# Optimization experiments

Measured on AMD Instinct MI355X. Metric: run time of the kernel, lower is better.

The kernel has to match this reference:

```python
import jax, jax.numpy as jnp
import numpy as np

D_MODEL = 1024
NUM_HEADS = 16
D_K = D_MODEL // NUM_HEADS
B, S = 1, 4096


def setup_inputs() -> dict:
    key = jax.random.key(0)
    ks = jax.random.split(key, 11)
    std = 1.0 / np.sqrt(D_MODEL)
    def lin(k):
        kw, kb = jax.random.split(k)
        W = jax.random.uniform(kw, (D_MODEL, D_MODEL), jnp.float32, -std, std)
        b = jax.random.uniform(kb, (D_MODEL,), jnp.float32, -std, std)
        return W, b
    Wq, bq = lin(ks[0]); Wk, bk = lin(ks[1]); Wv, bv = lin(ks[2]); Wo, bo = lin(ks[3])
    q = jax.random.normal(ks[4], (B, S, D_MODEL), jnp.float32)
    k = jax.random.normal(ks[5], (B, S, D_MODEL), jnp.float32)
    v = jax.random.normal(ks[6], (B, S, D_MODEL), jnp.float32)
    return {"q": q, "k": k, "v": v,
            "Wq": Wq, "bq": bq, "Wk": Wk, "bk": bk,
            "Wv": Wv, "bv": bv, "Wo": Wo, "bo": bo}


def reference(q, k, v, Wq, bq, Wk, bk, Wv, bv, Wo, bo):
    Bq, Sq, _ = q.shape
    # Linear projections (torch Linear: x @ W.T + b)
    def split_heads(x):
        return x.reshape(Bq, -1, NUM_HEADS, D_K).transpose(0, 2, 1, 3)  # [B,H,S,Dk]
    query = split_heads(q @ Wq.T + bq)
    key_ = split_heads(k @ Wk.T + bk)
    value = split_heads(v @ Wv.T + bv)
    scores = jnp.einsum('bhsd,bhtd->bhst', query, key_) / jnp.sqrt(jnp.float32(D_K))
    attn = jax.nn.softmax(scores, axis=-1)  # [B,H,S,S]
    ctx = jnp.einsum('bhst,bhtd->bhsd', attn, value)
    ctx = ctx.transpose(0, 2, 1, 3).reshape(Bq, Sq, NUM_HEADS * D_K)
    return ctx @ Wo.T + bo
```

## Files before the change

### kernel.cpp

```cpp
#include <hip/hip_runtime.h>
#include <cstdint>
#include <cstddef>

#define S_LEN 4096
#define DMODEL 1024
#define NHEADS 16
#define DK 64
#define ACT (S_LEN * DMODEL)
#define WELE (DMODEL * DMODEL)

typedef __bf16 bf16;
typedef bf16  bf16x4 __attribute__((ext_vector_type(4)));
typedef bf16  bf16x8 __attribute__((ext_vector_type(8)));
typedef float f32x4  __attribute__((ext_vector_type(4)));

__device__ __forceinline__ void async16(const void* g, void* l) {
    __builtin_amdgcn_global_load_lds(
        (__attribute__((address_space(1))) void*)(uintptr_t)g,
        (__attribute__((address_space(3))) void*)(uintptr_t)l,
        16, 0, 0);
}

__device__ __forceinline__ float fast_exp2(float x) {
#if __has_builtin(__builtin_amdgcn_exp2f)
    return __builtin_amdgcn_exp2f(x);
#else
    return exp2f(x);
#endif
}

__global__ void __launch_bounds__(256) cvt7(
    const float* a0, const float* a1, const float* a2,
    const float* w0, const float* w1, const float* w2, const float* w3,
    bf16* oa0, bf16* oa1, bf16* oa2,
    bf16* ow0, bf16* ow1, bf16* ow2, bf16* ow3,
    int nA, int nB)
{
    const float* s; bf16* d; int n4;
    switch (blockIdx.y) {
        case 0: s = a0; d = oa0; n4 = nA; break;
        case 1: s = a1; d = oa1; n4 = nA; break;
        case 2: s = a2; d = oa2; n4 = nA; break;
        case 3: s = w0; d = ow0; n4 = nB; break;
        case 4: s = w1; d = ow1; n4 = nB; break;
        case 5: s = w2; d = ow2; n4 = nB; break;
        default: s = w3; d = ow3; n4 = nB; break;
    }
    int i = blockIdx.x * 256 + threadIdx.x;
    if (i < n4) {
        float4 v = ((const float4*)s)[i];
        bf16x4 r = { (bf16)v.x, (bf16)v.y, (bf16)v.z, (bf16)v.w };
        ((bf16x4*)d)[i] = r;
    }
}

__device__ __forceinline__ void gemm_core_128x128(
    const bf16* __restrict__ A, const bf16* __restrict__ B,
    bf16* As, bf16* Bs, f32x4 (&acc)[4][4],
    int m0, int n0, int wm, int wn, int K)
{
    const int tid  = threadIdx.x;
    const int wave = tid >> 6;
    const int lane = tid & 63;
    const int quad = lane >> 4;
    const int l16  = lane & 15;

    const int srow = tid >> 2;
    const int scol = (tid & 3) * 8;
    const bf16* Ag = A + (size_t)(m0 + srow) * K + scol;
    const bf16* Bg = B + (size_t)(n0 + srow) * K + scol;
    char* lA = (char*)As + wave * 1024;
    char* lB = (char*)Bs + wave * 1024;

    for (int k0 = 0; k0 < K; k0 += 32) {
        async16(Ag,                  lA);
        async16(Ag + (size_t)64 * K, lA + 4096);
        async16(Bg,                  lB);
        async16(Bg + (size_t)64 * K, lB + 4096);
        Ag += 32; Bg += 32;
        __syncthreads();

        bf16x8 af[4], bfr[4];
#pragma unroll
        for (int i = 0; i < 4; ++i)
            af[i] = *(const bf16x8*)&As[(wm + i * 16 + l16) * 32 + quad * 8];
#pragma unroll
        for (int i = 0; i < 4; ++i)
            bfr[i] = *(const bf16x8*)&Bs[(wn + i * 16 + l16) * 32 + quad * 8];

#pragma unroll
        for (int mi = 0; mi < 4; ++mi)
#pragma unroll
            for (int ni = 0; ni < 4; ++ni)
                acc[mi][ni] = __builtin_amdgcn_mfma_f32_16x16x32_bf16(
                    af[mi], bfr[ni], acc[mi][ni], 0, 0, 0);
        __syncthreads();
    }
}

__global__ void __launch_bounds__(256) proj_qkv(
    const bf16* __restrict__ Xq, const bf16* __restrict__ Wq, const float* __restrict__ bq, bf16* __restrict__ Qo,
    const bf16* __restrict__ Xk, const bf16* __restrict__ Wk, const float* __restrict__ bk, bf16* __restrict__ Ko,
    const bf16* __restrict__ Xv, const bf16* __restrict__ Wv, const float* __restrict__ bv, bf16* __restrict__ Vo,
    float qscale)
{
    __shared__ __align__(16) bf16 As[128 * 32];
    __shared__ __align__(16) bf16 Bs[128 * 32];

    const int which = blockIdx.z;
    const bf16*  A    = (which == 0) ? Xq : (which == 1) ? Xk : Xv;
    const bf16*  Bw   = (which == 0) ? Wq : (which == 1) ? Wk : Wv;
    const float* bias = (which == 0) ? bq : (which == 1) ? bk : bv;
    const float  scale = (which == 0) ? qscale : 1.0f;

    const int tid  = threadIdx.x;
    const int wave = tid >> 6;
    const int lane = tid & 63;
    const int quad = lane >> 4;
    const int l16  = lane & 15;
    const int m0 = blockIdx.x * 128;
    const int n0 = blockIdx.y * 128;
    const int wm = (wave & 1) * 64;
    const int wn = (wave >> 1) * 64;

    f32x4 acc[4][4] = {};
    gemm_core_128x128(A, Bw, As, Bs, acc, m0, n0, wm, wn, DMODEL);

    if (which < 2) {
        bf16* out = (which == 0) ? Qo : Ko;
#pragma unroll
        for (int mi = 0; mi < 4; ++mi)
#pragma unroll
            for (int ni = 0; ni < 4; ++ni) {
                const int n = n0 + wn + ni * 16 + l16;
                const float bn = bias[n];
                const int dk = n & 63;
                const int cc = dk >> 3, ee = dk & 7;
                const size_t hb = (size_t)(n >> 6) * S_LEN * DK;
#pragma unroll
                for (int r = 0; r < 4; ++r) {
                    const int m = m0 + wm + mi * 16 + quad * 4 + r;
                    const int pdk = ((cc ^ (m & 7)) << 3) | ee;
                    out[hb + (size_t)m * DK + pdk] = (bf16)((acc[mi][ni][r] + bn) * scale);
                }
            }
    } else {
#pragma unroll
        for (int mi = 0; mi < 4; ++mi)
#pragma unroll
            for (int ni = 0; ni < 4; ++ni) {
                const int n = n0 + wn + ni * 16 + l16;
                const float bn = bias[n];
                const int dk = n & 63;
                const size_t hb = (size_t)(n >> 6) * (64 * S_LEN);
                const int mbase = m0 + wm + mi * 16 + quad * 4;
                const int T  = mbase >> 6;
                const int tt = mbase & 63;
                const int pos = (((tt >> 3) ^ (dk & 7)) << 3) | (tt & 7);
                bf16x4 r4;
#pragma unroll
                for (int r = 0; r < 4; ++r) r4[r] = (bf16)(acc[mi][ni][r] + bn);
                *(bf16x4*)&Vo[hb + (size_t)T * 4096 + dk * 64 + pos] = r4;
            }
    }
}

__global__ void __launch_bounds__(256) gemm_out(
    const bf16* __restrict__ A, const bf16* __restrict__ Bw,
    const float* __restrict__ bias, float* __restrict__ out)
{
    __shared__ __align__(16) bf16 As[128 * 32];
    __shared__ __align__(16) bf16 Bs[128 * 32];

    const int tid  = threadIdx.x;
    const int wave = tid >> 6;
    const int lane = tid & 63;
    const int quad = lane >> 4;
    const int l16  = lane & 15;
    const int m0 = blockIdx.x * 128;
    const int n0 = blockIdx.y * 128;
    const int wm = (wave & 1) * 64;
    const int wn = (wave >> 1) * 64;

    f32x4 acc[4][4] = {};
    gemm_core_128x128(A, Bw, As, Bs, acc, m0, n0, wm, wn, DMODEL);

#pragma unroll
    for (int mi = 0; mi < 4; ++mi)
#pragma unroll
        for (int ni = 0; ni < 4; ++ni) {
            const int n = n0 + wn + ni * 16 + l16;
            const float bn = bias[n];
#pragma unroll
            for (int r = 0; r < 4; ++r) {
                const int m = m0 + wm + mi * 16 + quad * 4 + r;
                out[(size_t)m * DMODEL + n] = acc[mi][ni][r] + bn;
            }
        }
}

__global__ void __launch_bounds__(128) flash_attn(
    const bf16* __restrict__ Q, const bf16* __restrict__ Kh,
    const bf16* __restrict__ Vt, bf16* __restrict__ ctx)
{
    __shared__ __align__(16) bf16 Qs[64 * 64];
    __shared__ __align__(16) bf16 Ks[64 * 64];
    __shared__ __align__(16) bf16 Vs[64 * 64];
    __shared__ __align__(16) bf16 Ps[2][32 * 68];

    const int tid  = threadIdx.x;
    const int wave = tid >> 6;
    const int lane = tid & 63;
    const int quad = lane >> 4;
    const int l16  = lane & 15;
    const int key8  = (quad ^ (l16 & 7)) << 3;
    const int key8b = key8 ^ 32;
    const int s0 = blockIdx.x * 64;
    const int h  = blockIdx.y;

    const bf16* Qg = Q  + (size_t)h * S_LEN * DK + (size_t)s0 * DK;
    const bf16* Kb = Kh + (size_t)h * S_LEN * DK;
    const bf16* Vb = Vt + (size_t)h * (64 * S_LEN);

#pragma unroll
    for (int j = 0; j < 4; ++j)
        async16(Qg + j * 1024 + tid * 8, (char*)Qs + wave * 1024 + j * 2048);
    __syncthreads();

    bf16x8 aq[2][2];
#pragma unroll
    for (int mi = 0; mi < 2; ++mi) {
        const bf16* qb = &Qs[(wave * 32 + mi * 16 + l16) * 64];
        aq[mi][0] = *(const bf16x8*)(qb + key8);
        aq[mi][1] = *(const bf16x8*)(qb + key8b);
    }

    f32x4 o[2][4] = {};
    f32x4 lsum4[2] = {};
    bf16* Pw = &Ps[wave][0];

    for (int t0 = 0; t0 < S_LEN; t0 += 64) {
        {
            const bf16* kg = Kb + (size_t)t0 * DK;
#pragma unroll
            for (int j = 0; j < 4; ++j)
                async16(kg + j * 1024 + tid * 8, (char*)Ks + wave * 1024 + j * 2048);
            const bf16* vg = Vb + (size_t)t0 * 64;
#pragma unroll
            for (int j = 0; j < 4; ++j)
                async16(vg + j * 1024 + tid * 8, (char*)Vs + wave * 1024 + j * 2048);
        }
        __syncthreads();

        f32x4 sc[2][4] = {};
#pragma unroll
        for (int ti = 0; ti < 4; ++ti) {
            const bf16* kp = &Ks[(ti * 16 + l16) * 64];
            bf16x8 bk0 = *(const bf16x8*)(kp + key8);
            bf16x8 bk1 = *(const bf16x8*)(kp + key8b);
#pragma unroll
            for (int mi = 0; mi < 2; ++mi) {
                sc[mi][ti] = __builtin_amdgcn_mfma_f32_16x16x32_bf16(bk0, aq[mi][0], sc[mi][ti], 0, 0, 0);
                sc[mi][ti] = __builtin_amdgcn_mfma_f32_16x16x32_bf16(bk1, aq[mi][1], sc[mi][ti], 0, 0, 0);
            }
        }

#pragma unroll
        for (int mi = 0; mi < 2; ++mi) {
            const int prow = (mi * 16 + l16) * 68;
#pragma unroll
            for (int ti = 0; ti < 4; ++ti) {
                f32x4 p;
#pragma unroll
                for (int r = 0; r < 4; ++r)
                    p[r] = fast_exp2(sc[mi][ti][r]);
                lsum4[mi] += p;
                bf16x4 pk = { (bf16)p[0], (bf16)p[1], (bf16)p[2], (bf16)p[3] };
                *(bf16x4*)&Pw[prow + ti * 16 + quad * 4] = pk;
            }
        }

#pragma unroll
        for (int mi = 0; mi < 2; ++mi) {
            const bf16* pb = &Pw[(mi * 16 + l16) * 68];
            bf16x4 p0a = *(const bf16x4*)(pb + quad * 8);
            bf16x4 p0b = *(const bf16x4*)(pb + quad * 8 + 4);
            bf16x4 p1a = *(const bf16x4*)(pb + 32 + quad * 8);
            bf16x4 p1b = *(const bf16x4*)(pb + 32 + quad * 8 + 4);
            bf16x8 ap0 = __builtin_shufflevector(p0a, p0b, 0, 1, 2, 3, 4, 5, 6, 7);
            bf16x8 ap1 = __builtin_shufflevector(p1a, p1b, 0, 1, 2, 3, 4, 5, 6, 7);
#pragma unroll
            for (int di = 0; di < 4; ++di) {
                const bf16* vp = &Vs[(di * 16 + l16) * 64];
                bf16x8 bv0 = *(const bf16x8*)(vp + key8);
                bf16x8 bv1 = *(const bf16x8*)(vp + key8b);
                o[mi][di] = __builtin_amdgcn_mfma_f32_16x16x32_bf16(bv0, ap0, o[mi][di], 0, 0, 0);
                o[mi][di] = __builtin_amdgcn_mfma_f32_16x16x32_bf16(bv1, ap1, o[mi][di], 0, 0, 0);
            }
        }
        __syncthreads();
    }

#pragma unroll
    for (int mi = 0; mi < 2; ++mi) {
        float ls = lsum4[mi][0] + lsum4[mi][1] + lsum4[mi][2] + lsum4[mi][3];
        ls += __shfl_xor(ls, 16);
        ls += __shfl_xor(ls, 32);
        const float rinv = 1.0f / ls;
        const int s = s0 + wave * 32 + mi * 16 + l16;
#pragma unroll
        for (int di = 0; di < 4; ++di) {
            bf16x4 r4 = { (bf16)(o[mi][di][0] * rinv), (bf16)(o[mi][di][1] * rinv),
                          (bf16)(o[mi][di][2] * rinv), (bf16)(o[mi][di][3] * rinv) };
            *(bf16x4*)&ctx[(size_t)s * DMODEL + h * DK + di * 16 + quad * 4] = r4;
        }
    }
}

extern "C" void kernel_launch(void* const* d_in, const int* in_sizes, int n_in,
                              void* d_out, int out_size, void* d_ws, size_t ws_size,
                              hipStream_t stream)
{
    (void)in_sizes; (void)n_in; (void)out_size; (void)ws_size;
    const float* q  = (const float*)d_in[0];
    const float* k  = (const float*)d_in[1];
    const float* v  = (const float*)d_in[2];
    const float* Wq = (const float*)d_in[3];
    const float* bq = (const float*)d_in[4];
    const float* Wk = (const float*)d_in[5];
    const float* bk = (const float*)d_in[6];
    const float* Wv = (const float*)d_in[7];
    const float* bv = (const float*)d_in[8];
    const float* Wo = (const float*)d_in[9];
    const float* bo = (const float*)d_in[10];

    bf16* Xq  = (bf16*)d_ws;
    bf16* Xk  = Xq  + ACT;
    bf16* Xv  = Xk  + ACT;
    bf16* Wqb = Xv  + ACT;
    bf16* Wkb = Wqb + WELE;
    bf16* Wvb = Wkb + WELE;
    bf16* Wob = Wvb + WELE;
    bf16* Qh  = Wob + WELE;
    bf16* Kh  = Qh  + ACT;
    bf16* Vt  = Kh  + ACT;
    bf16* CTX = Vt  + ACT;

    cvt7<<<dim3(ACT / 4 / 256, 7), 256, 0, stream>>>(
        q, k, v, Wq, Wk, Wv, Wo,
        Xq, Xk, Xv, Wqb, Wkb, Wvb, Wob, ACT / 4, WELE / 4);

    const float qscale = 0.125f * 1.4426950408889634f;
    proj_qkv<<<dim3(S_LEN / 128, DMODEL / 128, 3), 256, 0, stream>>>(
        Xq, Wqb, bq, Qh, Xk, Wkb, bk, Kh, Xv, Wvb, bv, Vt, qscale);

    flash_attn<<<dim3(S_LEN / 64, NHEADS), 128, 0, stream>>>(Qh, Kh, Vt, CTX);

    gemm_out<<<dim3(S_LEN / 128, DMODEL / 128), 256, 0, stream>>>(CTX, Wob, bo, (float*)d_out);
}
```

Measured before the change: 289.8 us.

## Use 32x32 MFMA with register-resident P in flash attention; shrink out-proj tile

Rewrites the flash attention inner loop to use 32x32x16 bf16 MFMAs, with Q fragments loaded straight from global memory into registers. The softmax probabilities are now rearranged between lane halves with a cross-lane shuffle instead of a round trip through an LDS P buffer, which drops the Qs and Ps shared arrays and their LDS traffic. The output projection GEMM moves to 64x128 tiles with its own inline load loop, giving twice as many blocks to fill the GPU. The risks are higher register pressure from the f32x16 accumulators and lower per-block reuse in the smaller GEMM tiles.

```diff
diff --git a/kernel.cpp b/kernel.cpp
--- a/kernel.cpp
+++ b/kernel.cpp
@@ -13,6 +13,7 @@
 typedef bf16  bf16x4 __attribute__((ext_vector_type(4)));
 typedef bf16  bf16x8 __attribute__((ext_vector_type(8)));
 typedef float f32x4  __attribute__((ext_vector_type(4)));
+typedef float f32x16 __attribute__((ext_vector_type(16)));
 
 __device__ __forceinline__ void async16(const void* g, void* l) {
     __builtin_amdgcn_global_load_lds(
@@ -169,7 +170,7 @@
     const bf16* __restrict__ A, const bf16* __restrict__ Bw,
     const float* __restrict__ bias, float* __restrict__ out)
 {
-    __shared__ __align__(16) bf16 As[128 * 32];
+    __shared__ __align__(16) bf16 As[64 * 32];
     __shared__ __align__(16) bf16 Bs[128 * 32];
 
     const int tid  = threadIdx.x;
@@ -177,16 +178,44 @@
     const int lane = tid & 63;
     const int quad = lane >> 4;
     const int l16  = lane & 15;
-    const int m0 = blockIdx.x * 128;
+    const int m0 = blockIdx.x * 64;
     const int n0 = blockIdx.y * 128;
-    const int wm = (wave & 1) * 64;
+    const int wm = (wave & 1) * 32;
     const int wn = (wave >> 1) * 64;
 
-    f32x4 acc[4][4] = {};
-    gemm_core_128x128(A, Bw, As, Bs, acc, m0, n0, wm, wn, DMODEL);
-
-#pragma unroll
-    for (int mi = 0; mi < 4; ++mi)
+    const int srow = tid >> 2;
+    const int scol = (tid & 3) * 8;
+    const bf16* Ag  = A  + (size_t)(m0 + srow) * DMODEL + scol;
+    const bf16* Bg  = Bw + (size_t)(n0 + srow) * DMODEL + scol;
+    const bf16* Bg2 = Bg + (size_t)64 * DMODEL;
+
+    f32x4 acc[2][4] = {};
+    for (int k0 = 0; k0 < DMODEL; k0 += 32) {
+        async16(Ag,  (char*)As + wave * 1024);
+        async16(Bg,  (char*)Bs + wave * 1024);
+        async16(Bg2, (char*)Bs + 4096 + wave * 1024);
+        Ag += 32; Bg += 32; Bg2 += 32;
+        __syncthreads();
+
+        bf16x8 af[2], bfr[4];
+#pragma unroll
+        for (int i = 0; i < 2; ++i)
+            af[i] = *(const bf16x8*)&As[(wm + i * 16 + l16) * 32 + quad * 8];
+#pragma unroll
+        for (int i = 0; i < 4; ++i)
+            bfr[i] = *(const bf16x8*)&Bs[(wn + i * 16 + l16) * 32 + quad * 8];
+
+#pragma unroll
+        for (int mi = 0; mi < 2; ++mi)
+#pragma unroll
+            for (int ni = 0; ni < 4; ++ni)
+                acc[mi][ni] = __builtin_amdgcn_mfma_f32_16x16x32_bf16(
+                    af[mi], bfr[ni], acc[mi][ni], 0, 0, 0);
+        __syncthreads();
+    }
+
+#pragma unroll
+    for (int mi = 0; mi < 2; ++mi)
 #pragma unroll
         for (int ni = 0; ni < 4; ++ni) {
             const int n = n0 + wn + ni * 16 + l16;
@@ -203,118 +232,96 @@
     const bf16* __restrict__ Q, const bf16* __restrict__ Kh,
     const bf16* __restrict__ Vt, bf16* __restrict__ ctx)
 {
-    __shared__ __align__(16) bf16 Qs[64 * 64];
     __shared__ __align__(16) bf16 Ks[64 * 64];
     __shared__ __align__(16) bf16 Vs[64 * 64];
-    __shared__ __align__(16) bf16 Ps[2][32 * 68];
 
     const int tid  = threadIdx.x;
     const int wave = tid >> 6;
     const int lane = tid & 63;
-    const int quad = lane >> 4;
-    const int l16  = lane & 15;
-    const int key8  = (quad ^ (l16 & 7)) << 3;
-    const int key8b = key8 ^ 32;
+    const int ln   = lane & 31;
+    const int lh   = lane >> 5;
+    const int e    = ln & 7;
     const int s0 = blockIdx.x * 64;
     const int h  = blockIdx.y;
 
-    const bf16* Qg = Q  + (size_t)h * S_LEN * DK + (size_t)s0 * DK;
-    const bf16* Kb = Kh + (size_t)h * S_LEN * DK;
-    const bf16* Vb = Vt + (size_t)h * (64 * S_LEN);
-
-#pragma unroll
-    for (int j = 0; j < 4; ++j)
-        async16(Qg + j * 1024 + tid * 8, (char*)Qs + wave * 1024 + j * 2048);
-    __syncthreads();
-
-    bf16x8 aq[2][2];
-#pragma unroll
-    for (int mi = 0; mi < 2; ++mi) {
-        const bf16* qb = &Qs[(wave * 32 + mi * 16 + l16) * 64];
-        aq[mi][0] = *(const bf16x8*)(qb + key8);
-        aq[mi][1] = *(const bf16x8*)(qb + key8b);
-    }
-
-    f32x4 o[2][4] = {};
-    f32x4 lsum4[2] = {};
-    bf16* Pw = &Ps[wave][0];
-
-    for (int t0 = 0; t0 < S_LEN; t0 += 64) {
-        {
-            const bf16* kg = Kb + (size_t)t0 * DK;
-#pragma unroll
-            for (int j = 0; j < 4; ++j)
-                async16(kg + j * 1024 + tid * 8, (char*)Ks + wave * 1024 + j * 2048);
-            const bf16* vg = Vb + (size_t)t0 * 64;
-#pragma unroll
-            for (int j = 0; j < 4; ++j)
-                async16(vg + j * 1024 + tid * 8, (char*)Vs + wave * 1024 + j * 2048);
-        }
-        __syncthreads();
-
-        f32x4 sc[2][4] = {};
-#pragma unroll
-        for (int ti = 0; ti < 4; ++ti) {
-            const bf16* kp = &Ks[(ti * 16 + l16) * 64];
-            bf16x8 bk0 = *(const bf16x8*)(kp + key8);
-            bf16x8 bk1 = *(const bf16x8*)(kp + key8b);
-#pragma unroll
-            for (int mi = 0; mi < 2; ++mi) {
-                sc[mi][ti] = __builtin_amdgcn_mfma_f32_16x16x32_bf16(bk0, aq[mi][0], sc[mi][ti], 0, 0, 0);
-                sc[mi][ti] = __builtin_amdgcn_mfma_f32_16x16x32_bf16(bk1, aq[mi][1], sc[mi][ti], 0, 0, 0);
-            }
-        }
-
-#pragma unroll
-        for (int mi = 0; mi < 2; ++mi) {
-            const int prow = (mi * 16 + l16) * 68;
-#pragma unroll
-            for (int ti = 0; ti < 4; ++ti) {
+    const bf16* qrow = Q + (size_t)h * S_LEN * DK + (size_t)(s0 + wave * 32 + ln) * DK;
+    bf16x8 bq[4];
+#pragma unroll
+    for (int kd = 0; kd < 4; ++kd)
+        bq[kd] = *(const bf16x8*)(qrow + (((kd * 2 + lh) ^ e) << 3));
+
+    const bf16* Kg = Kh + (size_t)h * S_LEN * DK + tid * 8;
+    const bf16* Vg = Vt + (size_t)h * (64 * S_LEN) + tid * 8;
+
+    f32x16 o[2] = {};
+    float lsum = 0.f;
+
+    for (int it = 0; it < 64; ++it) {
+#pragma unroll
+        for (int j = 0; j < 4; ++j) {
+            async16(Kg + j * 1024, (char*)Ks + wave * 1024 + j * 2048);
+            async16(Vg + j * 1024, (char*)Vs + wave * 1024 + j * 2048);
+        }
+        Kg += 4096; Vg += 4096;
+        __syncthreads();
+
+        f32x16 sc[2] = {};
+#pragma unroll
+        for (int kd = 0; kd < 4; ++kd) {
+            const int koff = ((kd * 2 + lh) ^ e) << 3;
+#pragma unroll
+            for (int tt = 0; tt < 2; ++tt) {
+                bf16x8 ak = *(const bf16x8*)&Ks[(tt * 32 + ln) * 64 + koff];
+                sc[tt] = __builtin_amdgcn_mfma_f32_32x32x16_bf16(ak, bq[kd], sc[tt], 0, 0, 0);
+            }
+        }
+
+        bf16x4 pk[2][4];
+#pragma unroll
+        for (int tt = 0; tt < 2; ++tt)
+#pragma unroll
+            for (int g4 = 0; g4 < 4; ++g4) {
                 f32x4 p;
 #pragma unroll
-                for (int r = 0; r < 4; ++r)
-                    p[r] = fast_exp2(sc[mi][ti][r]);
-                lsum4[mi] += p;
-                bf16x4 pk = { (bf16)p[0], (bf16)p[1], (bf16)p[2], (bf16)p[3] };
-                *(bf16x4*)&Pw[prow + ti * 16 + quad * 4] = pk;
-            }
-        }
-
-#pragma unroll
-        for (int mi = 0; mi < 2; ++mi) {
-            const bf16* pb = &Pw[(mi * 16 + l16) * 68];
-            bf16x4 p0a = *(const bf16x4*)(pb + quad * 8);
-            bf16x4 p0b = *(const bf16x4*)(pb + quad * 8 + 4);
-            bf16x4 p1a = *(const bf16x4*)(pb + 32 + quad * 8);
-            bf16x4 p1b = *(const bf16x4*)(pb + 32 + quad * 8 + 4);
-            bf16x8 ap0 = __builtin_shufflevector(p0a, p0b, 0, 1, 2, 3, 4, 5, 6, 7);
-            bf16x8 ap1 = __builtin_shufflevector(p1a, p1b, 0, 1, 2, 3, 4, 5, 6, 7);
-#pragma unroll
-            for (int di = 0; di < 4; ++di) {
-                const bf16* vp = &Vs[(di * 16 + l16) * 64];
-                bf16x8 bv0 = *(const bf16x8*)(vp + key8);
-                bf16x8 bv1 = *(const bf16x8*)(vp + key8b);
-                o[mi][di] = __builtin_amdgcn_mfma_f32_16x16x32_bf16(bv0, ap0, o[mi][di], 0, 0, 0);
-                o[mi][di] = __builtin_amdgcn_mfma_f32_16x16x32_bf16(bv1, ap1, o[mi][di], 0, 0, 0);
-            }
-        }
-        __syncthreads();
-    }
-
-#pragma unroll
-    for (int mi = 0; mi < 2; ++mi) {
-        float ls = lsum4[mi][0] + lsum4[mi][1] + lsum4[mi][2] + lsum4[mi][3];
-        ls += __shfl_xor(ls, 16);
-        ls += __shfl_xor(ls, 32);
-        const float rinv = 1.0f / ls;
-        const int s = s0 + wave * 32 + mi * 16 + l16;
-#pragma unroll
-        for (int di = 0; di < 4; ++di) {
-            bf16x4 r4 = { (bf16)(o[mi][di][0] * rinv), (bf16)(o[mi][di][1] * rinv),
-                          (bf16)(o[mi][di][2] * rinv), (bf16)(o[mi][di][3] * rinv) };
-            *(bf16x4*)&ctx[(size_t)s * DMODEL + h * DK + di * 16 + quad * 4] = r4;
-        }
-    }
+                for (int r = 0; r < 4; ++r) p[r] = fast_exp2(sc[tt][g4 * 4 + r]);
+                lsum += p[0] + p[1] + p[2] + p[3];
+                bf16x4 q4 = { (bf16)p[0], (bf16)p[1], (bf16)p[2], (bf16)p[3] };
+                pk[tt][g4] = q4;
+            }
+
+#pragma unroll
+        for (int kt = 0; kt < 4; ++kt) {
+            const int g = kt & 1, tt = kt >> 1;
+            union { bf16x4 v; unsigned long long u; } a, b, r_;
+            a.v = pk[tt][2 * g];
+            b.v = pk[tt][2 * g + 1];
+            unsigned long long send = lh ? a.u : b.u;
+            r_.u = __shfl_xor(send, 32);
+            union { bf16x8 v; unsigned long long u[2]; } bp;
+            bp.u[0] = lh ? r_.u : a.u;
+            bp.u[1] = lh ? b.u : r_.u;
+            const int voff = ((kt * 2 + lh) ^ e) << 3;
+#pragma unroll
+            for (int dt = 0; dt < 2; ++dt) {
+                bf16x8 av = *(const bf16x8*)&Vs[(dt * 32 + ln) * 64 + voff];
+                o[dt] = __builtin_amdgcn_mfma_f32_32x32x16_bf16(av, bp.v, o[dt], 0, 0, 0);
+            }
+        }
+        __syncthreads();
+    }
+
+    float ls = lsum + __shfl_xor(lsum, 32);
+    const float rinv = 1.0f / ls;
+    const int s = s0 + wave * 32 + ln;
+    bf16* crow = ctx + (size_t)s * DMODEL + h * DK;
+#pragma unroll
+    for (int dt = 0; dt < 2; ++dt)
+#pragma unroll
+        for (int g4 = 0; g4 < 4; ++g4) {
+            bf16x4 r4 = { (bf16)(o[dt][g4 * 4 + 0] * rinv), (bf16)(o[dt][g4 * 4 + 1] * rinv),
+                          (bf16)(o[dt][g4 * 4 + 2] * rinv), (bf16)(o[dt][g4 * 4 + 3] * rinv) };
+            *(bf16x4*)&crow[dt * 32 + g4 * 8 + lh * 4] = r4;
+        }
 }
 
 extern "C" void kernel_launch(void* const* d_in, const int* in_sizes, int n_in,
@@ -356,5 +363,5 @@
 
     flash_attn<<<dim3(S_LEN / 64, NHEADS), 128, 0, stream>>>(Qh, Kh, Vt, CTX);
 
-    gemm_out<<<dim3(S_LEN / 128, DMODEL / 128), 256, 0, stream>>>(CTX, Wob, bo, (float*)d_out);
-}
+    gemm_out<<<dim3(S_LEN / 64, DMODEL / 128), 256, 0, stream>>>(CTX, Wob, bo, (float*)d_out);
+}
```

New measurement: 309.6 us. 1.07x slower.
